# Kernel optimization log

Measured on AMD Instinct MI355X. Metric: run time of the kernel, lower is better.

## Reference

```python
import jax, jax.numpy as jnp
import numpy as np

B, S, D = 2, 2048, 1024
H, E = 16, 64


def setup_inputs() -> dict:
    key = jax.random.key(0)
    k1, k2, k3, k4 = jax.random.split(key, 4)
    x = jax.random.normal(k1, (B, S, D), dtype=jnp.float32)
    # per-head Q/K/V projection weights, stacked over the head axis
    scale = 1.0 / np.sqrt(D)
    Wq = jax.random.normal(k2, (H, D, E), dtype=jnp.float32) * scale
    Wk = jax.random.normal(k3, (H, D, E), dtype=jnp.float32) * scale
    Wv = jax.random.normal(k4, (H, D, E), dtype=jnp.float32) * scale
    return {"x": x, "Wq": Wq, "Wk": Wk, "Wv": Wv}


def reference(x, Wq, Wk, Wv):
    # Grouped-over-heads equivalent of the per-head torch loop.
    q = jnp.einsum("bsd,hde->bhse", x, Wq)  # [B,H,S,E]
    k = jnp.einsum("bsd,hde->bhse", x, Wk)
    v = jnp.einsum("bsd,hde->bhse", x, Wv)

    scores = jnp.einsum("bhse,bhte->bhst", q, k)  # [B,H,S,S]
    scores = scores / jnp.sqrt(jnp.asarray(E, dtype=scores.dtype))
    causal = jnp.tril(jnp.ones((S, S), dtype=bool))  # True on/below diagonal
    scores = jnp.where(causal, scores, jnp.finfo(scores.dtype).min)
    attn = jax.nn.softmax(scores, axis=-1)  # dropout p=0.0 -> identity

    out = jnp.einsum("bhst,bhte->bhse", attn, v)  # [B,H,S,E]
    # concat over heads on the last dim, matching torch.concat(..., dim=-1)
    return out.transpose(0, 2, 1, 3).reshape(B, S, H * E)
```

## Files before the change

kernel.cpp:

```cpp
#include <hip/hip_runtime.h>
#include <stdint.h>

#define S_LEN 2048
#define D_DIM 1024
#define NB 2
#define NH 16
#define NE 64
#define QK_COLS 2048
#define K_DIM D_DIM

typedef unsigned short u16;
typedef unsigned int u32;
typedef u16 u16x8 __attribute__((ext_vector_type(8)));
typedef __bf16 bf16x8 __attribute__((ext_vector_type(8)));
typedef float f32x4 __attribute__((ext_vector_type(4)));

__device__ __forceinline__ u16 f2b(float f) {
  u32 u = __builtin_bit_cast(u32, f);
  return (u16)((u + 0x7FFFu + ((u >> 16) & 1u)) >> 16);
}

__device__ __forceinline__ void gload_lds16(const void* g, void* l) {
  __builtin_amdgcn_global_load_lds(
      (const __attribute__((address_space(1))) u32*)g,
      (__attribute__((address_space(3))) u32*)l, 16, 0, 0);
}

__device__ __forceinline__ int sigma64(int m) {
  return (m & 32) | ((m & 12) << 1) | ((m & 16) >> 2) | (m & 3);
}

__global__ __launch_bounds__(256) void k_prep(const float* __restrict__ x,
                                              const float* __restrict__ Wq,
                                              const float* __restrict__ Wk,
                                              const float* __restrict__ Wv,
                                              u16* __restrict__ xb,
                                              u16* __restrict__ Wt) {
  __shared__ u16 tile[64][65];
  int bid = blockIdx.x;
  int t = threadIdx.x;
  if (bid < 2048) {
    size_t i = (size_t)bid * 256 + t;
    const float4* xf = (const float4*)x;
    float4 a = xf[2 * i], c = xf[2 * i + 1];
    u16x8 o;
    o[0] = f2b(a.x); o[1] = f2b(a.y); o[2] = f2b(a.z); o[3] = f2b(a.w);
    o[4] = f2b(c.x); o[5] = f2b(c.y); o[6] = f2b(c.z); o[7] = f2b(c.w);
    *(u16x8*)(xb + 8 * i) = o;
  } else {
    int wbid = bid - 2048;
    int kb = wbid & 15;
    int h = (wbid >> 4) & 15;
    int proj = wbid >> 8;
    const float* W = (proj == 0) ? Wq : ((proj == 1) ? Wk : Wv);
    int k0 = kb * 64;
    int e = t & 63, kr = t >> 6;
    const float* src = W + ((size_t)h * D_DIM + k0 + kr * 16) * NE + e;
#pragma unroll
    for (int j = 0; j < 16; ++j) tile[kr * 16 + j][e] = f2b(src[(size_t)j * NE]);
    __syncthreads();
    int e2 = t >> 2, kc = (t & 3) * 16;
    u16x8 o0, o1;
#pragma unroll
    for (int j = 0; j < 8; ++j) { o0[j] = tile[kc + j][e2]; o1[j] = tile[kc + 8 + j][e2]; }
    size_t n = (size_t)proj * 1024 + h * 64 + e2;
    u16* dst = Wt + n * K_DIM + k0 + kc;
    *(u16x8*)dst = o0;
    *(u16x8*)(dst + 8) = o1;
  }
}

__global__ __launch_bounds__(256) void k_gemm(const u16* __restrict__ A,
                                              const u16* __restrict__ Bt,
                                              u16* __restrict__ Cqk,
                                              u16* __restrict__ VT) {
  __shared__ __align__(16) u16 As[2][128 * 64];
  __shared__ __align__(16) u16 Bs[2][128 * 64];
  int t = threadIdx.x;
  int lane = t & 63, w = t >> 6;
  int hi = lane >> 4, l15 = lane & 15;
  int wr = (w >> 1) * 64, wc = (w & 1) * 64;
  int bid = blockIdx.x;
  int xcd = bid & 7, r0 = bid >> 3;
  int fam3 = r0 % 3;
  bool isV = (fam3 == 2);
  int m0, n0;
  const u16 *arows, *brows;
  if (!isV) {
    int qi = (r0 / 3) * 2 + fam3;
    m0 = (qi >> 1) * 128;
    n0 = (xcd * 2 + (qi & 1)) * 128;
    arows = A + (size_t)m0 * K_DIM;
    brows = Bt + (size_t)n0 * K_DIM;
  } else {
    m0 = xcd * 128;
    n0 = (r0 / 3) * 128;
    arows = Bt + (size_t)(2048 + m0) * K_DIM;
    brows = A + (size_t)n0 * K_DIM;
  }
  float qscale = (!isV && (n0 + wc) < 1024) ? 0.18033688f : 1.0f;
  f32x4 acc[4][4];
#pragma unroll
  for (int m = 0; m < 4; m++)
#pragma unroll
    for (int n = 0; n < 4; n++)
#pragma unroll
      for (int j = 0; j < 4; j++) acc[m][n][j] = 0.f;

  auto stage = [&](int buf, int k0) {
#pragma unroll
    for (int i = 0; i < 4; ++i) {
      int ci = i * 256 + t;
      int row = ci >> 3, c = ci & 7;
      int cs = c ^ (row & 7);
      gload_lds16(arows + (size_t)row * K_DIM + k0 + cs * 8,
                  (char*)As[buf] + (size_t)(i * 256 + w * 64) * 16);
      gload_lds16(brows + (size_t)row * K_DIM + k0 + cs * 8,
                  (char*)Bs[buf] + (size_t)(i * 256 + w * 64) * 16);
    }
  };

  stage(0, 0);
  __syncthreads();

  int cur = 0;
  for (int t64 = 0; t64 < 16; ++t64) {
    if (t64 < 15) stage(cur ^ 1, (t64 + 1) * 64);
#pragma unroll
    for (int ks = 0; ks < 2; ++ks) {
      int kc = ks * 4 + hi;
      bf16x8 af[4], bfr[4];
#pragma unroll
      for (int m = 0; m < 4; m++) {
        int r = wr + m * 16 + l15;
        af[m] = *(const bf16x8*)&As[cur][r * 64 + ((kc ^ (r & 7)) * 8)];
      }
#pragma unroll
      for (int n = 0; n < 4; n++) {
        int r = wc + n * 16 + l15;
        bfr[n] = *(const bf16x8*)&Bs[cur][r * 64 + ((kc ^ (r & 7)) * 8)];
      }
      __builtin_amdgcn_s_setprio(1);
#pragma unroll
      for (int m = 0; m < 4; m++)
#pragma unroll
        for (int n = 0; n < 4; n++)
          acc[m][n] = __builtin_amdgcn_mfma_f32_16x16x32_bf16(af[m], bfr[n], acc[m][n], 0, 0, 0);
      __builtin_amdgcn_s_setprio(0);
    }
    __syncthreads();
    cur ^= 1;
  }

  if (!isV) {
#pragma unroll
    for (int m = 0; m < 4; m++) {
#pragma unroll
      for (int r = 0; r < 4; r++) {
        int row = m0 + wr + m * 16 + hi * 4 + r;
#pragma unroll
        for (int n = 0; n < 4; n++) {
          int col = n0 + wc + n * 16 + l15;
          Cqk[(size_t)row * QK_COLS + col] = f2b(acc[m][n][r] * qscale);
        }
      }
    }
  } else {
#pragma unroll
    for (int m = 0; m < 4; m++) {
#pragma unroll
      for (int r = 0; r < 4; r++) {
        int vrow = m0 + wr + m * 16 + hi * 4 + r;
#pragma unroll
        for (int n = 0; n < 4; n++) {
          int col = n0 + wc + n * 16 + l15;
          VT[(size_t)((col >> 11) * 1024 + vrow) * S_LEN + (col & 2047)] =
              f2b(acc[m][n][r]);
        }
      }
    }
  }
}

__device__ __forceinline__ void stage_k(const u16* kb_, u16* kdst, int kv0, int t, int w) {
#pragma unroll
  for (int i = 0; i < 2; ++i) {
    int ci = i * 256 + t;
    int row = ci >> 3, c = ci & 7;
    int srow = sigma64(row);
    int cs = c ^ (row & 7);
    gload_lds16(kb_ + (size_t)(kv0 + srow) * QK_COLS + cs * 8,
                (char*)kdst + (size_t)(i * 256 + w * 64) * 16);
  }
}

__device__ __forceinline__ void stage_v(const u16* vtb_, u16* vdst, int kv0, int t, int w) {
#pragma unroll
  for (int i = 0; i < 2; ++i) {
    int ci = i * 256 + t;
    int row = ci >> 3, c = ci & 7;
    int cs = c ^ (row & 7);
    gload_lds16(vtb_ + (size_t)row * S_LEN + kv0 + cs * 8,
                (char*)vdst + (size_t)(i * 256 + w * 64) * 16);
  }
}

__global__ __launch_bounds__(256) void k_attn(const u16* __restrict__ qk,
                                              const u16* __restrict__ VT,
                                              float* __restrict__ out) {
  __shared__ __align__(16) u16 Ks[2][64 * 64];
  __shared__ __align__(16) u16 Vs[2][64 * 64];
  int t = threadIdx.x;
  int lane = t & 63, w = t >> 6;
  int hi = lane >> 4, l15 = lane & 15;
  int bid = blockIdx.x;
  int x = bid & 7, g = bid >> 3;
  int bh = x * 4 + (g & 3);
  int qt = 31 - (g >> 2);
  int b = bh >> 4, h = bh & 15;
  const u16* qb_ = qk + (size_t)b * S_LEN * QK_COLS + h * NE;
  const u16* kb_ = qb_ + 1024;
  const u16* vtb_ = VT + (size_t)bh * 64 * S_LEN;

  int q0 = qt * 64;
  int nt = qt + 1;
  int wqb = q0 + w * 16;

  bf16x8 qf[2];
#pragma unroll
  for (int ks = 0; ks < 2; ks++)
    qf[ks] = *(const bf16x8*)(qb_ + (size_t)(wqb + l15) * QK_COLS + ks * 32 + hi * 8);

  f32x4 o[4];
#pragma unroll
  for (int i = 0; i < 4; i++)
#pragma unroll
    for (int j = 0; j < 4; j++) o[i][j] = 0.f;
  float lsum = 0.f;
  int myq = wqb + l15;

  stage_k(kb_, Ks[0], 0, t, w);
  stage_v(vtb_, Vs[0], 0, t, w);
  __syncthreads();

  int cur = 0;
  for (int ti = 0; ti < nt; ++ti) {
    int kv0 = ti * 64;
    bool pf = (ti + 1 < nt);
    if (pf) {
      stage_k(kb_, Ks[cur ^ 1], kv0 + 64, t, w);
      stage_v(vtb_, Vs[cur ^ 1], kv0 + 64, t, w);
    }

    f32x4 s[4];
#pragma unroll
    for (int f = 0; f < 4; f++)
#pragma unroll
      for (int j = 0; j < 4; j++) s[f][j] = 0.f;
    __builtin_amdgcn_s_setprio(1);
#pragma unroll
    for (int ks = 0; ks < 2; ks++) {
      int kc = ks * 4 + hi;
#pragma unroll
      for (int f = 0; f < 4; f++) {
        int r = f * 16 + l15;
        bf16x8 kf = *(const bf16x8*)&Ks[cur][r * 64 + ((kc ^ (r & 7)) * 8)];
        s[f] = __builtin_amdgcn_mfma_f32_16x16x32_bf16(kf, qf[ks], s[f], 0, 0, 0);
      }
    }
    __builtin_amdgcn_s_setprio(0);

    bool diag = (ti == nt - 1);
#pragma unroll
    for (int f = 0; f < 4; f++) {
#pragma unroll
      for (int r = 0; r < 4; r++) {
        float p = __builtin_amdgcn_exp2f(s[f][r]);
        if (diag) {
          int kv = kv0 + sigma64(16 * f + 4 * hi + r);
          p = (kv <= myq) ? p : 0.f;
        }
        s[f][r] = p;
        lsum += p;
      }
    }

    __builtin_amdgcn_s_setprio(1);
#pragma unroll
    for (int ks = 0; ks < 2; ks++) {
      bf16x8 pa;
#pragma unroll
      for (int j = 0; j < 4; j++) {
        pa[j] = (__bf16)s[2 * ks][j];
        pa[4 + j] = (__bf16)s[2 * ks + 1][j];
      }
#pragma unroll
      for (int ef = 0; ef < 4; ef++) {
        int e = ef * 16 + l15;
        bf16x8 vbf = *(const bf16x8*)&Vs[cur][e * 64 + (((4 * ks + hi) ^ (e & 7)) * 8)];
        o[ef] = __builtin_amdgcn_mfma_f32_16x16x32_bf16(pa, vbf, o[ef], 0, 0, 0);
      }
    }
    __builtin_amdgcn_s_setprio(0);
    __syncthreads();
    cur ^= 1;
  }

  lsum += __shfl_xor(lsum, 16);
  lsum += __shfl_xor(lsum, 32);
#pragma unroll
  for (int r = 0; r < 4; r++) {
    float l = __shfl(lsum, 4 * hi + r);
    float inv = 1.0f / l;
    int q = wqb + 4 * hi + r;
#pragma unroll
    for (int ef = 0; ef < 4; ef++) {
      int col = h * NE + ef * 16 + l15;
      out[((size_t)b * S_LEN + q) * (NH * NE) + col] = o[ef][r] * inv;
    }
  }
}

extern "C" void kernel_launch(void* const* d_in, const int* in_sizes, int n_in,
                              void* d_out, int out_size, void* d_ws, size_t ws_size,
                              hipStream_t stream) {
  const float* x = (const float*)d_in[0];
  const float* Wq = (const float*)d_in[1];
  const float* Wk = (const float*)d_in[2];
  const float* Wv = (const float*)d_in[3];
  float* out = (float*)d_out;

  char* ws = (char*)d_ws;
  u16* xb = (u16*)ws;
  u16* Wt = (u16*)(ws + (8u << 20));
  u16* qk = (u16*)(ws + (14u << 20));
  u16* VT = (u16*)(ws + (30u << 20));

  k_prep<<<dim3(2816), dim3(256), 0, stream>>>(x, Wq, Wk, Wv, xb, Wt);
  k_gemm<<<dim3(768), dim3(256), 0, stream>>>(xb, Wt, qk, VT);
  k_attn<<<dim3(1024), dim3(256), 0, stream>>>(qk, VT, out);
}
```

Baseline: 84.61 us.

## Load V fragments directly from global into registers instead of staging in LDS

Removes the LDS double-buffer for V and has each lane load its V^T MFMA fragments straight from global memory at the start of each KV tile, issued before the QK^T MFMAs so the latency can overlap. This halves LDS usage and removes the V staging instructions. In exchange, each of the four waves loads the same V tile redundantly from global or L2, with 16-byte loads strided by the sequence length, and the load latency is exposed inside the iteration rather than prefetched a tile ahead.

Measured after the change: 129.7 us. 1.53x slower.

```diff
diff --git a/kernel.cpp b/kernel.cpp
--- a/kernel.cpp
+++ b/kernel.cpp
@@ -194,22 +194,10 @@
   }
 }
 
-__device__ __forceinline__ void stage_v(const u16* vtb_, u16* vdst, int kv0, int t, int w) {
-#pragma unroll
-  for (int i = 0; i < 2; ++i) {
-    int ci = i * 256 + t;
-    int row = ci >> 3, c = ci & 7;
-    int cs = c ^ (row & 7);
-    gload_lds16(vtb_ + (size_t)row * S_LEN + kv0 + cs * 8,
-                (char*)vdst + (size_t)(i * 256 + w * 64) * 16);
-  }
-}
-
 __global__ __launch_bounds__(256) void k_attn(const u16* __restrict__ qk,
                                               const u16* __restrict__ VT,
                                               float* __restrict__ out) {
   __shared__ __align__(16) u16 Ks[2][64 * 64];
-  __shared__ __align__(16) u16 Vs[2][64 * 64];
   int t = threadIdx.x;
   int lane = t & 63, w = t >> 6;
   int hi = lane >> 4, l15 = lane & 15;
@@ -239,18 +227,26 @@
   float lsum = 0.f;
   int myq = wqb + l15;
 
+  const u16* vrow_base[4];
+#pragma unroll
+  for (int ef = 0; ef < 4; ef++)
+    vrow_base[ef] = vtb_ + (size_t)(ef * 16 + l15) * S_LEN + 8 * hi;
+
   stage_k(kb_, Ks[0], 0, t, w);
-  stage_v(vtb_, Vs[0], 0, t, w);
   __syncthreads();
 
   int cur = 0;
   for (int ti = 0; ti < nt; ++ti) {
     int kv0 = ti * 64;
     bool pf = (ti + 1 < nt);
-    if (pf) {
-      stage_k(kb_, Ks[cur ^ 1], kv0 + 64, t, w);
-      stage_v(vtb_, Vs[cur ^ 1], kv0 + 64, t, w);
-    }
+    if (pf) stage_k(kb_, Ks[cur ^ 1], kv0 + 64, t, w);
+
+    bf16x8 vpre[2][4];
+#pragma unroll
+    for (int ks = 0; ks < 2; ks++)
+#pragma unroll
+      for (int ef = 0; ef < 4; ef++)
+        vpre[ks][ef] = *(const bf16x8*)(vrow_base[ef] + kv0 + 32 * ks);
 
     f32x4 s[4];
 #pragma unroll
@@ -295,11 +291,8 @@
         pa[4 + j] = (__bf16)s[2 * ks + 1][j];
       }
 #pragma unroll
-      for (int ef = 0; ef < 4; ef++) {
-        int e = ef * 16 + l15;
-        bf16x8 vbf = *(const bf16x8*)&Vs[cur][e * 64 + (((4 * ks + hi) ^ (e & 7)) * 8)];
-        o[ef] = __builtin_amdgcn_mfma_f32_16x16x32_bf16(pa, vbf, o[ef], 0, 0, 0);
-      }
+      for (int ef = 0; ef < 4; ef++)
+        o[ef] = __builtin_amdgcn_mfma_f32_16x16x32_bf16(pa, vpre[ks][ef], o[ef], 0, 0, 0);
     }
     __builtin_amdgcn_s_setprio(0);
     __syncthreads();
```
